# Optimization experiments

Hardware: AMD Instinct MI355X
Metric: run time of the kernel (lower is better)

Reference implementation:

```python
import jax, jax.numpy as jnp
import numpy as np

INPUT = 28
HIDDEN = 64
OUT = 10


def setup_inputs() -> dict:
    key = jax.random.key(0)
    ks = jax.random.split(key, 7)
    B = 65536
    bound_rnn = 1.0 / np.sqrt(HIDDEN)
    bound_fc = 1.0 / np.sqrt(HIDDEN)
    return {
        "x": jax.random.normal(ks[0], (B, 28, 28), dtype=jnp.float32),
        "w_ih": jax.random.uniform(ks[1], (HIDDEN, INPUT), jnp.float32, -bound_rnn, bound_rnn),
        "w_hh": jax.random.uniform(ks[2], (HIDDEN, HIDDEN), jnp.float32, -bound_rnn, bound_rnn),
        "b_ih": jax.random.uniform(ks[3], (HIDDEN,), jnp.float32, -bound_rnn, bound_rnn),
        "b_hh": jax.random.uniform(ks[4], (HIDDEN,), jnp.float32, -bound_rnn, bound_rnn),
        "fc_w": jax.random.uniform(ks[5], (OUT, HIDDEN), jnp.float32, -bound_fc, bound_fc),
        "fc_b": jax.random.uniform(ks[6], (OUT,), jnp.float32, -bound_fc, bound_fc),
    }


def reference(x, w_ih, w_hh, b_ih, b_hh, fc_w, fc_b):
    # Faithful to the torch source: hx is never updated inside the loop, so
    # every iteration recomputes rnn(x[:, s, :], zeros) and only the last
    # timestep's result survives. Equivalent math, computed once:
    x = x.reshape(-1, 28, 28)
    hx = jnp.zeros((x.shape[0], HIDDEN), dtype=x.dtype)
    inp = x[:, 27, :]  # [B, 28]
    h = jnp.tanh(inp @ w_ih.T + b_ih + hx @ w_hh.T + b_hh)  # [B, 64]
    return h @ fc_w.T + fc_b  # [B, 10]
```

## Files before the change

kernel.cpp:

```cpp
#include <hip/hip_runtime.h>
#include <math.h>

#define INPUT  28
#define HIDDEN 64
#define NOUT   10
#define BLK    256

__global__ __launch_bounds__(BLK) void rnn_fused(
    const float* __restrict__ x,
    const float* __restrict__ w_ih,
    const float* __restrict__ b_ih,
    const float* __restrict__ b_hh,
    const float* __restrict__ fc_w,
    const float* __restrict__ fc_b,
    float* __restrict__ out,
    int B)
{
    __shared__ float s_wih[HIDDEN * INPUT];
    __shared__ float s_fcw[HIDDEN * NOUT];
    __shared__ float s_bias[HIDDEN];
    __shared__ float s_fcb[NOUT];

    const int t = threadIdx.x;

    for (int i = t; i < HIDDEN * INPUT; i += BLK) s_wih[i] = w_ih[i];
    for (int i = t; i < HIDDEN * NOUT; i += BLK) {
        int h = i / NOUT, o = i - h * NOUT;
        s_fcw[i] = fc_w[o * HIDDEN + h];
    }
    if (t < HIDDEN) s_bias[t] = b_ih[t] + b_hh[t];
    if (t < NOUT)   s_fcb[t]  = fc_b[t];
    __syncthreads();

    const int b = blockIdx.x * BLK + t;
    if (b >= B) return;

    float inp[INPUT];
    const float4* xp = reinterpret_cast<const float4*>(x + (size_t)b * 784 + 756);
    #pragma unroll
    for (int k = 0; k < 7; ++k) {
        float4 v = xp[k];
        inp[4*k+0] = v.x; inp[4*k+1] = v.y; inp[4*k+2] = v.z; inp[4*k+3] = v.w;
    }

    float acc[NOUT];
    #pragma unroll
    for (int o = 0; o < NOUT; ++o) acc[o] = s_fcb[o];

    #pragma unroll 4
    for (int h = 0; h < HIDDEN; ++h) {
        float s = s_bias[h];
        #pragma unroll
        for (int c = 0; c < INPUT; ++c)
            s = fmaf(s_wih[h * INPUT + c], inp[c], s);
        const float th = tanhf(s);
        #pragma unroll
        for (int o = 0; o < NOUT; ++o)
            acc[o] = fmaf(s_fcw[h * NOUT + o], th, acc[o]);
    }

    float* op = out + (size_t)b * NOUT;
    #pragma unroll
    for (int o = 0; o < NOUT; ++o) op[o] = acc[o];
}

extern "C" void kernel_launch(void* const* d_in, const int* in_sizes, int n_in,
                              void* d_out, int out_size, void* d_ws, size_t ws_size,
                              hipStream_t stream)
{
    const float* x    = (const float*)d_in[0];
    const float* w_ih = (const float*)d_in[1];
    const float* b_ih = (const float*)d_in[3];
    const float* b_hh = (const float*)d_in[4];
    const float* fc_w = (const float*)d_in[5];
    const float* fc_b = (const float*)d_in[6];
    float* out = (float*)d_out;

    const int B = in_sizes[0] / (28 * 28);
    const int grid = (B + BLK - 1) / BLK;
    rnn_fused<<<grid, BLK, 0, stream>>>(x, w_ih, b_ih, b_hh, fc_w, fc_b, out, B);
}
```

Measured before the change: 263.6 us.

## Split hidden units across two thread halves and drop shared weight staging

Each block now handles 128 batch rows with 256 threads. Each half of the block computes 32 of the 64 hidden units, and the halves combine their partial outputs through shared memory. Weights are read directly from global memory as wave-uniform scalar loads instead of being staged in LDS, and tanhf is replaced by an exp-based formula. The aim is more parallelism per row and less LDS traffic and staging cost. In exchange, each thread loads its input row twice, a block-wide sync is added, and the bounds check on B is removed.

Result: no change. 265.5 us (+0.7%).

```diff
diff --git a/kernel.cpp b/kernel.cpp
--- a/kernel.cpp
+++ b/kernel.cpp
@@ -1,12 +1,12 @@
 #include <hip/hip_runtime.h>
-#include <math.h>
 
 #define INPUT  28
 #define HIDDEN 64
 #define NOUT   10
 #define BLK    256
+#define BPB    128
 
-__global__ __launch_bounds__(BLK) void rnn_fused(
+__global__ __launch_bounds__(BLK) void rnn_fused2(
     const float* __restrict__ x,
     const float* __restrict__ w_ih,
     const float* __restrict__ b_ih,
@@ -16,24 +16,12 @@
     float* __restrict__ out,
     int B)
 {
-    __shared__ float s_wih[HIDDEN * INPUT];
-    __shared__ float s_fcw[HIDDEN * NOUT];
-    __shared__ float s_bias[HIDDEN];
-    __shared__ float s_fcb[NOUT];
+    __shared__ float s_red[BPB][NOUT];
 
-    const int t = threadIdx.x;
-
-    for (int i = t; i < HIDDEN * INPUT; i += BLK) s_wih[i] = w_ih[i];
-    for (int i = t; i < HIDDEN * NOUT; i += BLK) {
-        int h = i / NOUT, o = i - h * NOUT;
-        s_fcw[i] = fc_w[o * HIDDEN + h];
-    }
-    if (t < HIDDEN) s_bias[t] = b_ih[t] + b_hh[t];
-    if (t < NOUT)   s_fcb[t]  = fc_b[t];
-    __syncthreads();
-
-    const int b = blockIdx.x * BLK + t;
-    if (b >= B) return;
+    const int t    = threadIdx.x;
+    const int bl   = t & (BPB - 1);
+    const int half = t >> 7;
+    const int b    = blockIdx.x * BPB + bl;
 
     float inp[INPUT];
     const float4* xp = reinterpret_cast<const float4*>(x + (size_t)b * 784 + 756);
@@ -45,23 +33,37 @@
 
     float acc[NOUT];
     #pragma unroll
-    for (int o = 0; o < NOUT; ++o) acc[o] = s_fcb[o];
+    for (int o = 0; o < NOUT; ++o) acc[o] = 0.0f;
 
-    #pragma unroll 4
-    for (int h = 0; h < HIDDEN; ++h) {
-        float s = s_bias[h];
+    const int h0 = half * (HIDDEN / 2);
+    #pragma unroll 2
+    for (int hh = 0; hh < HIDDEN / 2; ++hh) {
+        const int h = h0 + hh;
+        float s = b_ih[h] + b_hh[h];
+        const float* wr = w_ih + h * INPUT;
         #pragma unroll
         for (int c = 0; c < INPUT; ++c)
-            s = fmaf(s_wih[h * INPUT + c], inp[c], s);
-        const float th = tanhf(s);
+            s = fmaf(wr[c], inp[c], s);
+
+        float e  = __expf(2.0f * s);
+        float th = 1.0f - 2.0f / (e + 1.0f);
+
         #pragma unroll
         for (int o = 0; o < NOUT; ++o)
-            acc[o] = fmaf(s_fcw[h * NOUT + o], th, acc[o]);
+            acc[o] = fmaf(fc_w[o * HIDDEN + h], th, acc[o]);
     }
 
-    float* op = out + (size_t)b * NOUT;
-    #pragma unroll
-    for (int o = 0; o < NOUT; ++o) op[o] = acc[o];
+    if (half == 1) {
+        #pragma unroll
+        for (int o = 0; o < NOUT; ++o) s_red[bl][o] = acc[o];
+    }
+    __syncthreads();
+    if (half == 0) {
+        float* op = out + (size_t)b * NOUT;
+        #pragma unroll
+        for (int o = 0; o < NOUT; ++o)
+            op[o] = acc[o] + s_red[bl][o] + fc_b[o];
+    }
 }
 
 extern "C" void kernel_launch(void* const* d_in, const int* in_sizes, int n_in,
@@ -77,6 +79,6 @@
     float* out = (float*)d_out;
 
     const int B = in_sizes[0] / (28 * 28);
-    const int grid = (B + BLK - 1) / BLK;
-    rnn_fused<<<grid, BLK, 0, stream>>>(x, w_ih, b_ih, b_hh, fc_w, fc_b, out, B);
+    const int grid = (B + BPB - 1) / BPB;
+    rnn_fused2<<<grid, BLK, 0, stream>>>(x, w_ih, b_ih, b_hh, fc_w, fc_b, out, B);
 }
```
